# Optimization experiments

Measured on AMD Instinct MI355X. Metric: run time of the kernel, lower is better.

Reference implementation:

```python
import jax, jax.numpy as jnp
import numpy as np

LN_EPS = 1e-5

def _layer_norm(x, g, b):
    m = jnp.mean(x, axis=-1, keepdims=True)
    v = jnp.mean((x - m) ** 2, axis=-1, keepdims=True)
    return (x - m) / jnp.sqrt(v + LN_EPS) * g + b

def setup_inputs() -> dict:
    key = jax.random.key(0)
    ks = jax.random.split(key, 16)
    B, L, D = 4, 2048, 1024
    DF = 4 * D
    s_in = 1.0 / np.sqrt(D)
    s_ff = 1.0 / np.sqrt(DF)
    # torch init of phazor: exp(2j*pi*arange(D)/D) * |randn|
    ang = 2.0 * np.pi * jnp.arange(D, dtype=jnp.float32) / D
    mag = jnp.abs(jax.random.normal(ks[0], (D,), jnp.float32))
    return {
        "x": jax.random.normal(ks[1], (B, L, D), jnp.float32),
        "hidden_real": jax.random.normal(ks[2], (B, D), jnp.float32),
        "hidden_imag": jax.random.normal(ks[3], (B, D), jnp.float32),
        "phazor_real": mag * jnp.cos(ang),
        "phazor_imag": mag * jnp.sin(ang),
        "phazor_init_real": jax.random.normal(ks[4], (D,), jnp.float32),
        "phazor_init_imag": jax.random.normal(ks[5], (D,), jnp.float32),
        "ln_gamma": jnp.ones((D,), jnp.float32),
        "ln_beta": jnp.zeros((D,), jnp.float32),
        "fc_w": jax.random.uniform(ks[6], (D, D), jnp.float32, -s_in, s_in),
        "fc_b": jax.random.uniform(ks[7], (D,), jnp.float32, -s_in, s_in),
        "w1": jax.random.uniform(ks[8], (DF, D), jnp.float32, -s_in, s_in),
        "b1": jax.random.uniform(ks[9], (DF,), jnp.float32, -s_in, s_in),
        "w2": jax.random.uniform(ks[10], (D, DF), jnp.float32, -s_ff, s_ff),
        "b2": jax.random.uniform(ks[11], (D,), jnp.float32, -s_ff, s_ff),
    }

def _spiral_conv(x, hidden, phazor_p, phazor_init):
    # x: [B,L,D] real, hidden: [B,D] complex
    B, L, D = x.shape
    amag = jnp.abs(phazor_p)
    phazor = phazor_p / amag * jnp.exp(-amag)                      # [D]
    prog = jnp.power(phazor[None, :], jnp.arange(L)[:, None])      # [L,D]
    filt = prog * phazor_init[None, :]                             # [L,D]
    filt_fft = jnp.fft.fft(filt, n=2 * L, axis=0)                  # [2L,D]
    x_fft = jnp.fft.fft(x.astype(jnp.complex64), n=2 * L, axis=1)  # [B,2L,D]
    conv = jnp.fft.ifft(filt_fft[None] * x_fft, axis=1)[:, :L]     # [B,L,D]
    conv_with_past = conv + jax.lax.stop_gradient(hidden)[:, None, :] * prog[None] * phazor[None, None]
    return conv_with_past.real, conv_with_past

def reference(x, hidden_real, hidden_imag, phazor_real, phazor_imag,
              phazor_init_real, phazor_init_imag, ln_gamma, ln_beta,
              fc_w, fc_b, w1, b1, w2, b2):
    hidden = hidden_real + 1j * hidden_imag
    phazor_p = phazor_real + 1j * phazor_imag
    phazor_init = phazor_init_real + 1j * phazor_init_imag

    x_res = x
    xn = _layer_norm(x, ln_gamma, ln_beta)
    s, new_hidden = _spiral_conv(xn, hidden, phazor_p, phazor_init)
    y = jax.nn.silu(jnp.einsum('bld,ed->ble', x, fc_w) + fc_b)
    h = s * y + x_res                      # dropout is identity (p=0 / eval)
    hn = _layer_norm(h, ln_gamma, ln_beta) # same LayerNorm instance reused
    ffn = jnp.einsum('blf,df->bld', jax.nn.silu(jnp.einsum('bld,fd->blf', hn, w1) + b1), w2) + b2
    out = ffn + h
    return out, new_hidden
```

## Files before the change

kernel.cpp:

```cpp
#include <hip/hip_runtime.h>

typedef unsigned short u16;
typedef unsigned int u32;
typedef float f32x4 __attribute__((ext_vector_type(4)));
typedef __bf16 bf16x8 __attribute__((ext_vector_type(8)));

__device__ __forceinline__ float b2f(u16 u) {
    return __uint_as_float(((u32)u) << 16);
}
__device__ __forceinline__ u16 f2b(float f) {
    u32 u = __float_as_uint(f);
    return (u16)((u + 0x7FFFu + ((u >> 16) & 1u)) >> 16);
}
__device__ __forceinline__ bool is_f32(const u32* flag) {
    return flag[0] == 0x3F800000u;
}
__device__ __forceinline__ float lda(const void* p, size_t i, bool f) {
    return f ? ((const float*)p)[i] : b2f(((const u16*)p)[i]);
}
__device__ __forceinline__ void cmul(float& xr, float& xi, float yr, float yi) {
    float tr = xr * yr - xi * yi;
    xi = xr * yi + xi * yr;
    xr = tr;
}
__device__ __forceinline__ void gl2lds16(const void* g, void* l) {
    __builtin_amdgcn_global_load_lds(
        (const __attribute__((address_space(1))) void*)g,
        (__attribute__((address_space(3))) void*)l, 16, 0, 0);
}
__device__ __forceinline__ void wg_barrier() {
    asm volatile("" ::: "memory");
    __builtin_amdgcn_sched_barrier(0);
    __builtin_amdgcn_s_barrier();
    __builtin_amdgcn_sched_barrier(0);
    asm volatile("" ::: "memory");
}
#define VWAIT0 { asm volatile("s_waitcnt vmcnt(0)" ::: "memory"); __builtin_amdgcn_sched_barrier(0); }
#define VWAIT2 { asm volatile("s_waitcnt vmcnt(2)" ::: "memory"); __builtin_amdgcn_sched_barrier(0); }
#define VWAIT4 { asm volatile("s_waitcnt vmcnt(4)" ::: "memory"); __builtin_amdgcn_sched_barrier(0); }
#define LGKM0  { asm volatile("s_waitcnt lgkmcnt(0)" ::: "memory"); __builtin_amdgcn_sched_barrier(0); }

__global__ __launch_bounds__(256) void cvt_k(const void* __restrict__ src,
                                             u32* __restrict__ dst, int n2,
                                             const u32* __restrict__ flag) {
    bool f = is_f32(flag);
    int i = blockIdx.x * 256 + threadIdx.x;
    if (i >= n2) return;
    if (f) {
        float2 v = ((const float2*)src)[i];
        dst[i] = (u32)f2b(v.x) | ((u32)f2b(v.y) << 16);
    } else {
        dst[i] = ((const u32*)src)[i];
    }
}

__global__ __launch_bounds__(256) void ln_k(const u16* __restrict__ x,
                                            const u16* __restrict__ g,
                                            const u16* __restrict__ be,
                                            u16* __restrict__ o, int D) {
    int row = blockIdx.x;
    const u16* xr = x + (size_t)row * D;
    int tid = threadIdx.x;
    float s = 0.f, s2 = 0.f;
    for (int i = tid; i < D; i += 256) {
        float v = b2f(xr[i]);
        s += v; s2 += v * v;
    }
    for (int off = 32; off > 0; off >>= 1) {
        s  += __shfl_down(s,  off, 64);
        s2 += __shfl_down(s2, off, 64);
    }
    __shared__ float red[8];
    int wave = tid >> 6;
    if ((tid & 63) == 0) { red[wave * 2] = s; red[wave * 2 + 1] = s2; }
    __syncthreads();
    if (tid == 0) {
        float ts = 0.f, ts2 = 0.f;
        for (int w = 0; w < 4; w++) { ts += red[w * 2]; ts2 += red[w * 2 + 1]; }
        float m = ts / D;
        float v = ts2 / D - m * m;
        red[0] = m;
        red[1] = rsqrtf(v + 1e-5f);
    }
    __syncthreads();
    float m = red[0], inv = red[1];
    u16* orow = o + (size_t)row * D;
    for (int i = tid; i < D; i += 256) {
        float v = (b2f(xr[i]) - m) * inv * b2f(g[i]) + b2f(be[i]);
        orow[i] = f2b(v);
    }
}

__global__ __launch_bounds__(256) void scan_partial_k(const u16* __restrict__ xn,
                                                      const void* __restrict__ phr_,
                                                      const void* __restrict__ phi_,
                                                      float2* __restrict__ T,
                                                      int L, int D, int C, int Kc,
                                                      const u32* __restrict__ flag) {
    bool f = is_f32(flag);
    int tid = blockIdx.x * 256 + threadIdx.x;
    int d = tid % D;
    int c = (tid / D) % C;
    int b = tid / (D * C);
    float pr = lda(phr_, d, f), pi = lda(phi_, d, f);
    float amag = fmaxf(sqrtf(pr * pr + pi * pi), 1e-12f);
    float sc = __expf(-amag) / amag;
    float phr = pr * sc, phi = pi * sc;
    float Tr = 0.f, Ti = 0.f;
    const u16* xp = xn + ((size_t)b * L + (size_t)c * Kc) * D + d;
    for (int t = 0; t < Kc; t++) {
        float x = b2f(xp[(size_t)t * D]);
        float nr = phr * Tr - phi * Ti + x;
        Ti = phr * Ti + phi * Tr;
        Tr = nr;
    }
    T[tid] = make_float2(Tr, Ti);
}

__global__ __launch_bounds__(256) void scan_prefix_k(const void* __restrict__ phr_,
                                                     const void* __restrict__ phi_,
                                                     const float2* __restrict__ T,
                                                     float2* __restrict__ E,
                                                     int D, int C,
                                                     const u32* __restrict__ flag) {
    bool f = is_f32(flag);
    int tid = blockIdx.x * 256 + threadIdx.x;
    int d = tid % D;
    int b = tid / D;
    float pr = lda(phr_, d, f), pi = lda(phi_, d, f);
    float amag = fmaxf(sqrtf(pr * pr + pi * pi), 1e-12f);
    float sc = __expf(-amag) / amag;
    float phr = pr * sc, phi = pi * sc;
    float kr = phr, ki = phi;
    for (int s = 0; s < 7; s++) cmul(kr, ki, kr, ki);
    float cr = 0.f, ci = 0.f;
    for (int c = 0; c < C; c++) {
        size_t i = ((size_t)b * C + c) * D + d;
        E[i] = make_float2(cr, ci);
        float2 t = T[i];
        cmul(cr, ci, kr, ki);
        cr += t.x; ci += t.y;
    }
}

__global__ __launch_bounds__(256) void scan_final_k(const u16* __restrict__ xn,
                                                    const void* __restrict__ phr_,
                                                    const void* __restrict__ phi_,
                                                    const void* __restrict__ pir_,
                                                    const void* __restrict__ pii_,
                                                    const void* __restrict__ hr_,
                                                    const void* __restrict__ hi_,
                                                    const float2* __restrict__ E,
                                                    u16* __restrict__ sws,
                                                    void* __restrict__ dout,
                                                    int MD, int out_elems,
                                                    int L, int D, int C, int Kc,
                                                    const u32* __restrict__ flag) {
    bool f = is_f32(flag);
    int tid = blockIdx.x * 256 + threadIdx.x;
    int d = tid % D;
    int c = (tid / D) % C;
    int b = tid / (D * C);
    float pr = lda(phr_, d, f), pi = lda(phi_, d, f);
    float amag = fmaxf(sqrtf(pr * pr + pi * pi), 1e-12f);
    float sc = __expf(-amag) / amag;
    float phr = pr * sc, phi = pi * sc;
    float kr = phr, ki = phi;
    for (int s = 0; s < 7; s++) cmul(kr, ki, kr, ki);
    float Pr = phr, Pi = phi;
    for (int j = 0; j < c; j++) cmul(Pr, Pi, kr, ki);
    float ir = lda(pir_, d, f), ii = lda(pii_, d, f);
    float hr = lda(hr_, (size_t)b * D + d, f), hi = lda(hi_, (size_t)b * D + d, f);
    float2 e = E[tid];
    float Sr = e.x, Si = e.y;
    const bool full = (out_elems >= 3 * MD);
    size_t mbase = (size_t)b * L + (size_t)c * Kc;
    for (int t = 0; t < Kc; t++) {
        size_t off = (mbase + t) * D + d;
        float x = b2f(xn[off]);
        float nr = phr * Sr - phi * Si + x;
        Si = phr * Si + phi * Sr;
        Sr = nr;
        float cr = ir * Sr - ii * Si + hr * Pr - hi * Pi;
        float ci = ir * Si + ii * Sr + hr * Pi + hi * Pr;
        sws[off] = f2b(cr);
        if (f) {
            float* fo = (float*)dout;
            if (full) {
                fo[(size_t)MD + 2 * off]     = cr;
                fo[(size_t)MD + 2 * off + 1] = ci;
            } else {
                fo[(size_t)MD + off] = cr;
            }
        } else {
            u16* uo = (u16*)dout;
            if (full) {
                uo[(size_t)MD + 2 * off]     = f2b(cr);
                uo[(size_t)MD + 2 * off + 1] = f2b(ci);
            } else {
                uo[(size_t)MD + off] = f2b(cr);
            }
        }
        cmul(Pr, Pi, phr, phi);
    }
}

template <int MODE, int BN>
__global__ __launch_bounds__(512) void gemm_nt(const u16* __restrict__ A,
                                               const u16* __restrict__ Bm,
                                               int M, int N, int K,
                                               const u16* __restrict__ bias,
                                               const u16* __restrict__ sbuf,
                                               const u16* __restrict__ xbuf,
                                               u16* __restrict__ out,
                                               void* __restrict__ outv,
                                               const u32* __restrict__ flag) {
    constexpr int WN = BN / 4;
    constexpr int NB = BN / 64;
    __shared__ u16 As[2][256 * 64];
    __shared__ u16 Bs[2][BN * 64];
    const int tid = threadIdx.x;
    const int wave = tid >> 6, lane = tid & 63;
    const int quad = lane >> 4, l16 = lane & 15;

    const int NT = N / BN;
    const int j = blockIdx.x;
    const int gsize = 8 * NT;
    const int mg  = j / gsize;
    const int rem = j - mg * gsize;
    const int nt  = rem >> 3;
    const int mi  = rem & 7;
    const int bm = (mg * 8 + mi) * 256, bn = nt * BN;

    const int wrow = (wave >> 2) * 128, wcol = (wave & 3) * WN;

    f32x4 acc[8][NB] = {};

    const int lr = lane >> 3;
    const int sl = (lane & 7) ^ lr;
    const size_t goff = (size_t)lr * K + sl * 8;
    const u16* aG = A  + (size_t)(bm + wave * 16) * K + goff;
    const u16* bG = Bm + (size_t)(bn + wave * 16) * K + goff;
    const size_t K8 = (size_t)K * 8;

#define STG_A(B_, t_, h_) { \
        const u16* ga = aG + (size_t)(t_) * 64 + (size_t)(h_) * 128 * K; \
        gl2lds16(ga,      &As[B_][((h_) * 128 + wave * 16) * 64]); \
        gl2lds16(ga + K8, &As[B_][((h_) * 128 + wave * 16 + 8) * 64]); }
#define STG_B(B_, t_, h_) { \
        const u16* gb = bG + (size_t)(t_) * 64 + (size_t)(h_) * 128 * K; \
        gl2lds16(gb,      &Bs[B_][((h_) * 128 + wave * 16) * 64]); \
        gl2lds16(gb + K8, &Bs[B_][((h_) * 128 + wave * 16 + 8) * 64]); }

#define RDA(B_, m_, ks_) (*(const bf16x8*)&As[B_][(wrow + (m_) * 16 + l16) * 64 + \
        ((((ks_) * 4 + quad) ^ (l16 & 7)) << 3)])
#define RDB(B_, n_, ks_) (*(const bf16x8*)&Bs[B_][(wcol + (n_) * 16 + l16) * 64 + \
        ((((ks_) * 4 + quad) ^ (l16 & 7)) << 3)])

#define LDA4(RB, mh) { \
        av[0][0] = RDA(RB, (mh) * 4 + 0, 0); av[0][1] = RDA(RB, (mh) * 4 + 0, 1); \
        av[1][0] = RDA(RB, (mh) * 4 + 1, 0); av[1][1] = RDA(RB, (mh) * 4 + 1, 1); \
        av[2][0] = RDA(RB, (mh) * 4 + 2, 0); av[2][1] = RDA(RB, (mh) * 4 + 2, 1); \
        av[3][0] = RDA(RB, (mh) * 4 + 3, 0); av[3][1] = RDA(RB, (mh) * 4 + 3, 1); }
#define LDB2(RB, nh) { \
        bv[(nh) * 2 + 0][0] = RDB(RB, (nh) * 2 + 0, 0); \
        bv[(nh) * 2 + 0][1] = RDB(RB, (nh) * 2 + 0, 1); \
        bv[(nh) * 2 + 1][0] = RDB(RB, (nh) * 2 + 1, 0); \
        bv[(nh) * 2 + 1][1] = RDB(RB, (nh) * 2 + 1, 1); }

#define FM(mi_, ni_, ks_) acc[mi_][ni_] = __builtin_amdgcn_mfma_f32_16x16x32_bf16( \
        av[(mi_) & 3][ks_], bv[ni_][ks_], acc[mi_][ni_], 0, 0, 0)
#define MFMA16(mh, nh) { \
        __builtin_amdgcn_s_setprio(1); \
        FM((mh)*4+0, (nh)*2+0, 0); FM((mh)*4+0, (nh)*2+1, 0); \
        FM((mh)*4+1, (nh)*2+0, 0); FM((mh)*4+1, (nh)*2+1, 0); \
        FM((mh)*4+2, (nh)*2+0, 0); FM((mh)*4+2, (nh)*2+1, 0); \
        FM((mh)*4+3, (nh)*2+0, 0); FM((mh)*4+3, (nh)*2+1, 0); \
        FM((mh)*4+0, (nh)*2+0, 1); FM((mh)*4+0, (nh)*2+1, 1); \
        FM((mh)*4+1, (nh)*2+0, 1); FM((mh)*4+1, (nh)*2+1, 1); \
        FM((mh)*4+2, (nh)*2+0, 1); FM((mh)*4+2, (nh)*2+1, 1); \
        FM((mh)*4+3, (nh)*2+0, 1); FM((mh)*4+3, (nh)*2+1, 1); \
        __builtin_amdgcn_s_setprio(0); }

    bf16x8 av[4][2], bv[NB][2];
    const int KT = K >> 6;

    if constexpr (BN == 256) {
        STG_A(0, 0, 0); STG_B(0, 0, 0); STG_B(0, 0, 1); STG_A(0, 0, 1);
        VWAIT4; wg_barrier();
#define TILE256(RB, SB, t_) { \
        const bool stg = (t_) + 1 < KT; \
         \
        LDA4(RB, 0); LDB2(RB, 0); \
        if (stg) STG_A(SB, (t_) + 1, 0);       \
        wg_barrier(); LGKM0; \
        MFMA16(0, 0); \
        if (stg) { VWAIT4 } else { VWAIT2 }    \
        wg_barrier(); \
         \
        LDB2(RB, 1); \
        if (stg) STG_B(SB, (t_) + 1, 0);       \
        wg_barrier(); LGKM0; \
        MFMA16(0, 1); \
        if (stg) { VWAIT4 } else { VWAIT0 }    \
        wg_barrier(); \
         \
        LDA4(RB, 1); \
        if (stg) STG_B(SB, (t_) + 1, 1);       \
        wg_barrier(); LGKM0; \
        MFMA16(1, 0); \
        wg_barrier(); \
         \
        if (stg) STG_A(SB, (t_) + 1, 1);       \
        wg_barrier(); LGKM0; \
        MFMA16(1, 1); \
        if (stg) { VWAIT4 }                    \
        wg_barrier(); }
        for (int t = 0; t < KT; t += 2) {
            TILE256(0, 1, t);
            TILE256(1, 0, t + 1);
        }
#undef TILE256
    } else {
        STG_B(0, 0, 0); STG_A(0, 0, 0); STG_A(0, 0, 1);
        VWAIT2; wg_barrier();
#define TILE128(RB, SB, t_) { \
        const bool stg = (t_) + 1 < KT; \
         \
        LDA4(RB, 0); LDB2(RB, 0); \
        if (stg) { STG_B(SB, (t_) + 1, 0); STG_A(SB, (t_) + 1, 0); }  \
        wg_barrier(); LGKM0; \
        MFMA16(0, 0); \
        if (stg) { VWAIT4 } else { VWAIT0 }    \
        wg_barrier(); \
         \
        LDA4(RB, 1); \
        if (stg) STG_A(SB, (t_) + 1, 1);       \
        wg_barrier(); LGKM0; \
        MFMA16(1, 0); \
        if (stg) { VWAIT2 }                    \
        wg_barrier(); }
        for (int t = 0; t < KT; t += 2) {
            TILE128(0, 1, t);
            TILE128(1, 0, t + 1);
        }
#undef TILE128
    }

    bool f = (MODE == 2) ? is_f32(flag) : false;
#pragma unroll
    for (int m = 0; m < 8; m++) {
#pragma unroll
        for (int n = 0; n < NB; n++) {
            int colg = bn + wcol + n * 16 + l16;
            float bsv = b2f(bias[colg]);
#pragma unroll
            for (int r = 0; r < 4; r++) {
                int rowg = bm + wrow + m * 16 + quad * 4 + r;
                size_t idx = (size_t)rowg * N + colg;
                float v = acc[m][n][r] + bsv;
                if (MODE == 0) {
                    float y = v / (1.f + __expf(-v));
                    float hv = b2f(sbuf[idx]) * y + b2f(xbuf[idx]);
                    out[idx] = f2b(hv);
                } else if (MODE == 1) {
                    float y = v / (1.f + __expf(-v));
                    out[idx] = f2b(y);
                } else {
                    float o = v + b2f(xbuf[idx]);
                    if (f) ((float*)outv)[idx] = o;
                    else   ((u16*)outv)[idx] = f2b(o);
                }
            }
        }
    }
#undef STG_A
#undef STG_B
#undef RDA
#undef RDB
#undef LDA4
#undef LDB2
#undef FM
#undef MFMA16
}

extern "C" void kernel_launch(void* const* d_in, const int* in_sizes, int n_in,
                              void* d_out, int out_size, void* d_ws, size_t ws_size,
                              hipStream_t stream) {
    const void* x   = d_in[0];
    const void* hr  = d_in[1];
    const void* hi  = d_in[2];
    const void* phr = d_in[3];
    const void* phi = d_in[4];
    const void* pir = d_in[5];
    const void* pii = d_in[6];
    const void* g   = d_in[7];
    const void* be  = d_in[8];
    const void* fcw = d_in[9];
    const void* fcb = d_in[10];
    const void* w1  = d_in[11];
    const void* b1  = d_in[12];
    const void* w2  = d_in[13];
    const void* b2  = d_in[14];
    const u32* flag = (const u32*)g;

    const int D  = in_sizes[3];
    const int Bb = in_sizes[1] / D;
    const int L  = in_sizes[0] / (Bb * D);
    const int DF = in_sizes[12];
    const int M  = Bb * L;
    const int Kc = 128, C = L / Kc;
    const int MD = M * D;

    char* ws = (char*)d_ws;
    size_t MD2 = (size_t)MD * 2;
    u16*    xb  = (u16*)(ws);
    u16*    xn  = (u16*)(ws + MD2);
    u16*    sws = (u16*)(ws + 2 * MD2);
    float2* T   = (float2*)(ws + 3 * MD2);
    float2* E   = (float2*)(ws + 3 * MD2 + (size_t)Bb * C * D * 8);
    u16*    a1  = (u16*)(ws);
    u16*    h   = (u16*)(ws + 4 * MD2);
    u16*    hn  = (u16*)(ws + 5 * MD2);
    char*   wp  = ws + 6 * MD2;
    u16* fcwb = (u16*)wp; wp += (size_t)D * D * 2;
    u16* w1b  = (u16*)wp; wp += (size_t)DF * D * 2;
    u16* w2b  = (u16*)wp; wp += (size_t)D * DF * 2;
    u16* fcbb = (u16*)wp; wp += (size_t)D * 2;
    u16* b1b  = (u16*)wp; wp += (size_t)DF * 2;
    u16* b2b  = (u16*)wp; wp += (size_t)D * 2;
    u16* gb   = (u16*)wp; wp += (size_t)D * 2;
    u16* bb   = (u16*)wp; wp += (size_t)D * 2;

    auto cvt = [&](const void* src, u16* dst, size_t n) {
        int n2 = (int)(n / 2);
        cvt_k<<<(n2 + 255) / 256, 256, 0, stream>>>(src, (u32*)dst, n2, flag);
    };
    cvt(x,   xb,   (size_t)MD);
    cvt(fcw, fcwb, (size_t)D * D);
    cvt(w1,  w1b,  (size_t)DF * D);
    cvt(w2,  w2b,  (size_t)D * DF);
    cvt(fcb, fcbb, (size_t)D);
    cvt(b1,  b1b,  (size_t)DF);
    cvt(b2,  b2b,  (size_t)D);
    cvt(g,   gb,   (size_t)D);
    cvt(be,  bb,   (size_t)D);

    ln_k<<<M, 256, 0, stream>>>(xb, gb, bb, xn, D);
    scan_partial_k<<<(Bb * C * D) / 256, 256, 0, stream>>>(xn, phr, phi, T, L, D, C, Kc, flag);
    scan_prefix_k<<<(Bb * D) / 256, 256, 0, stream>>>(phr, phi, T, E, D, C, flag);
    scan_final_k<<<(Bb * C * D) / 256, 256, 0, stream>>>(xn, phr, phi, pir, pii, hr, hi,
                                                         E, sws, d_out, MD, out_size,
                                                         L, D, C, Kc, flag);
    gemm_nt<0, 128><<<(M / 256) * (D / 128), 512, 0, stream>>>(xb, fcwb, M, D, D, fcbb, sws, xb, h, nullptr, flag);
    ln_k<<<M, 256, 0, stream>>>(h, gb, bb, hn, D);
    gemm_nt<1, 256><<<(M / 256) * (DF / 256), 512, 0, stream>>>(hn, w1b, M, DF, D, b1b, nullptr, nullptr, a1, nullptr, flag);
    gemm_nt<2, 128><<<(M / 256) * (D / 128), 512, 0, stream>>>(a1, w2b, M, D, DF, b2b, nullptr, h, nullptr, d_out, flag);
}
```

Measured before the change: 466.4 us.

## Triple-buffer BN=128 GEMM path and merge conversion launches into one kernel

The BN=128 GEMM variant now uses a 2x4 wave grid with 64x64 per-wave tiles and a three-stage LDS ring, so loads are issued two K-tiles ahead instead of one. This is meant to hide more global-load latency in the fc and w2 GEMMs. It costs more LDS per block, which may lower occupancy, and the new buffer rotation is more complex. Separately, the nine conversion kernel launches become a single multi-segment kernel. That removes launch overhead but adds a per-thread segment search loop.

```diff
diff --git a/kernel.cpp b/kernel.cpp
--- a/kernel.cpp
+++ b/kernel.cpp
@@ -38,19 +38,27 @@
 #define VWAIT0 { asm volatile("s_waitcnt vmcnt(0)" ::: "memory"); __builtin_amdgcn_sched_barrier(0); }
 #define VWAIT2 { asm volatile("s_waitcnt vmcnt(2)" ::: "memory"); __builtin_amdgcn_sched_barrier(0); }
 #define VWAIT4 { asm volatile("s_waitcnt vmcnt(4)" ::: "memory"); __builtin_amdgcn_sched_barrier(0); }
+#define VWAIT6 { asm volatile("s_waitcnt vmcnt(6)" ::: "memory"); __builtin_amdgcn_sched_barrier(0); }
 #define LGKM0  { asm volatile("s_waitcnt lgkmcnt(0)" ::: "memory"); __builtin_amdgcn_sched_barrier(0); }
 
-__global__ __launch_bounds__(256) void cvt_k(const void* __restrict__ src,
-                                             u32* __restrict__ dst, int n2,
-                                             const u32* __restrict__ flag) {
+struct CvtArgs {
+    const void* src[9];
+    u16* dst[9];
+    int n2[9];
+    int tot;
+};
+__global__ __launch_bounds__(256) void cvtm_k(CvtArgs a, const u32* __restrict__ flag) {
     bool f = is_f32(flag);
     int i = blockIdx.x * 256 + threadIdx.x;
-    if (i >= n2) return;
+    if (i >= a.tot) return;
+    int s = 0, base = 0;
+    while (i - base >= a.n2[s]) { base += a.n2[s]; s++; }
+    int k = i - base;
     if (f) {
-        float2 v = ((const float2*)src)[i];
-        dst[i] = (u32)f2b(v.x) | ((u32)f2b(v.y) << 16);
+        float2 v = ((const float2*)a.src[s])[k];
+        ((u32*)a.dst[s])[k] = (u32)f2b(v.x) | ((u32)f2b(v.y) << 16);
     } else {
-        dst[i] = ((const u32*)src)[i];
+        ((u32*)a.dst[s])[k] = ((const u32*)a.src[s])[k];
     }
 }
 
@@ -215,10 +223,10 @@
                                                u16* __restrict__ out,
                                                void* __restrict__ outv,
                                                const u32* __restrict__ flag) {
-    constexpr int WN = BN / 4;
-    constexpr int NB = BN / 64;
-    __shared__ u16 As[2][256 * 64];
-    __shared__ u16 Bs[2][BN * 64];
+    constexpr int NBUF = (BN == 256) ? 2 : 3;
+    constexpr int MR   = (BN == 256) ? 8 : 4;
+    __shared__ u16 As[NBUF][256 * 64];
+    __shared__ u16 Bs[NBUF][BN * 64];
     const int tid = threadIdx.x;
     const int wave = tid >> 6, lane = tid & 63;
     const int quad = lane >> 4, l16 = lane & 15;
@@ -232,16 +240,17 @@
     const int mi  = rem & 7;
     const int bm = (mg * 8 + mi) * 256, bn = nt * BN;
 
-    const int wrow = (wave >> 2) * 128, wcol = (wave & 3) * WN;
-
-    f32x4 acc[8][NB] = {};
+    const int wrow = (BN == 256) ? (wave >> 2) * 128 : (wave >> 1) * 64;
+    const int wcol = (BN == 256) ? (wave & 3) * 64   : (wave & 1) * 64;
+
+    f32x4 acc[MR][4] = {};
 
     const int lr = lane >> 3;
     const int sl = (lane & 7) ^ lr;
     const size_t goff = (size_t)lr * K + sl * 8;
-    const u16* aG = A  + (size_t)(bm + wave * 16) * K + goff;
+    const size_t K8 = (size_t)K * 8;
+    const u16* aG = A  + (size_t)(bm + ((BN == 256) ? wave * 16 : wave * 32)) * K + goff;
     const u16* bG = Bm + (size_t)(bn + wave * 16) * K + goff;
-    const size_t K8 = (size_t)K * 8;
 
 #define STG_A(B_, t_, h_) { \
         const u16* ga = aG + (size_t)(t_) * 64 + (size_t)(h_) * 128 * K; \
@@ -251,6 +260,16 @@
         const u16* gb = bG + (size_t)(t_) * 64 + (size_t)(h_) * 128 * K; \
         gl2lds16(gb,      &Bs[B_][((h_) * 128 + wave * 16) * 64]); \
         gl2lds16(gb + K8, &Bs[B_][((h_) * 128 + wave * 16 + 8) * 64]); }
+#define STG_A128(B_, t_) { \
+        const u16* ga = aG + (size_t)(t_) * 64; \
+        gl2lds16(ga,          &As[B_][(wave * 32) * 64]); \
+        gl2lds16(ga + K8,     &As[B_][(wave * 32 + 8) * 64]); \
+        gl2lds16(ga + 2 * K8, &As[B_][(wave * 32 + 16) * 64]); \
+        gl2lds16(ga + 3 * K8, &As[B_][(wave * 32 + 24) * 64]); }
+#define STG_B128(B_, t_) { \
+        const u16* gb = bG + (size_t)(t_) * 64; \
+        gl2lds16(gb,      &Bs[B_][(wave * 16) * 64]); \
+        gl2lds16(gb + K8, &Bs[B_][(wave * 16 + 8) * 64]); }
 
 #define RDA(B_, m_, ks_) (*(const bf16x8*)&As[B_][(wrow + (m_) * 16 + l16) * 64 + \
         ((((ks_) * 4 + quad) ^ (l16 & 7)) << 3)])
@@ -281,8 +300,15 @@
         FM((mh)*4+2, (nh)*2+0, 1); FM((mh)*4+2, (nh)*2+1, 1); \
         FM((mh)*4+3, (nh)*2+0, 1); FM((mh)*4+3, (nh)*2+1, 1); \
         __builtin_amdgcn_s_setprio(0); }
-
-    bf16x8 av[4][2], bv[NB][2];
+#define MFMA16K(ks_) { \
+        __builtin_amdgcn_s_setprio(1); \
+        FM(0, 0, ks_); FM(0, 1, ks_); FM(1, 0, ks_); FM(1, 1, ks_); \
+        FM(0, 2, ks_); FM(0, 3, ks_); FM(1, 2, ks_); FM(1, 3, ks_); \
+        FM(2, 0, ks_); FM(2, 1, ks_); FM(3, 0, ks_); FM(3, 1, ks_); \
+        FM(2, 2, ks_); FM(2, 3, ks_); FM(3, 2, ks_); FM(3, 3, ks_); \
+        __builtin_amdgcn_s_setprio(0); }
+
+    bf16x8 av[4][2], bv[4][2];
     const int KT = K >> 6;
 
     if constexpr (BN == 256) {
@@ -322,36 +348,45 @@
         }
 #undef TILE256
     } else {
-        STG_B(0, 0, 0); STG_A(0, 0, 0); STG_A(0, 0, 1);
-        VWAIT2; wg_barrier();
+        STG_A128(0, 0); STG_B128(0, 0);
+        STG_A128(1, 1); STG_B128(1, 1);
+        VWAIT6;
+        wg_barrier();
 #define TILE128(RB, SB, t_) { \
-        const bool stg = (t_) + 1 < KT; \
-         \
-        LDA4(RB, 0); LDB2(RB, 0); \
-        if (stg) { STG_B(SB, (t_) + 1, 0); STG_A(SB, (t_) + 1, 0); }  \
-        wg_barrier(); LGKM0; \
-        MFMA16(0, 0); \
-        if (stg) { VWAIT4 } else { VWAIT0 }    \
+        const bool stg = (t_) + 2 < KT; \
+         \
+        av[0][0] = RDA(RB, 0, 0); av[1][0] = RDA(RB, 1, 0); \
+        av[2][0] = RDA(RB, 2, 0); av[3][0] = RDA(RB, 3, 0); \
+        bv[0][0] = RDB(RB, 0, 0); bv[1][0] = RDB(RB, 1, 0); \
+        bv[2][0] = RDB(RB, 2, 0); bv[3][0] = RDB(RB, 3, 0); \
+        if (stg) STG_A128(SB, (t_) + 2); \
+        wg_barrier(); LGKM0; \
+        MFMA16K(0); \
         wg_barrier(); \
          \
-        LDA4(RB, 1); \
-        if (stg) STG_A(SB, (t_) + 1, 1);       \
-        wg_barrier(); LGKM0; \
-        MFMA16(1, 0); \
-        if (stg) { VWAIT2 }                    \
+        av[0][1] = RDA(RB, 0, 1); av[1][1] = RDA(RB, 1, 1); \
+        av[2][1] = RDA(RB, 2, 1); av[3][1] = RDA(RB, 3, 1); \
+        bv[0][1] = RDB(RB, 0, 1); bv[1][1] = RDB(RB, 1, 1); \
+        bv[2][1] = RDB(RB, 2, 1); bv[3][1] = RDB(RB, 3, 1); \
+        if (stg) STG_B128(SB, (t_) + 2); \
+        wg_barrier(); LGKM0; \
+        MFMA16K(1); \
+        if (stg) { VWAIT6 }                    \
+        else if ((t_) + 1 < KT) { VWAIT0 }     \
         wg_barrier(); }
-        for (int t = 0; t < KT; t += 2) {
-            TILE128(0, 1, t);
-            TILE128(1, 0, t + 1);
+        for (int t = 0; t < KT; t += 3) {
+            TILE128(0, 2, t);
+            if (t + 1 < KT) TILE128(1, 0, t + 1);
+            if (t + 2 < KT) TILE128(2, 1, t + 2);
         }
 #undef TILE128
     }
 
     bool f = (MODE == 2) ? is_f32(flag) : false;
 #pragma unroll
-    for (int m = 0; m < 8; m++) {
+    for (int m = 0; m < MR; m++) {
 #pragma unroll
-        for (int n = 0; n < NB; n++) {
+        for (int n = 0; n < 4; n++) {
             int colg = bn + wcol + n * 16 + l16;
             float bsv = b2f(bias[colg]);
 #pragma unroll
@@ -376,12 +411,15 @@
     }
 #undef STG_A
 #undef STG_B
+#undef STG_A128
+#undef STG_B128
 #undef RDA
 #undef RDB
 #undef LDA4
 #undef LDB2
 #undef FM
 #undef MFMA16
+#undef MFMA16K
 }
 
 extern "C" void kernel_launch(void* const* d_in, const int* in_sizes, int n_in,
@@ -432,19 +470,20 @@
     u16* gb   = (u16*)wp; wp += (size_t)D * 2;
     u16* bb   = (u16*)wp; wp += (size_t)D * 2;
 
-    auto cvt = [&](const void* src, u16* dst, size_t n) {
-        int n2 = (int)(n / 2);
-        cvt_k<<<(n2 + 255) / 256, 256, 0, stream>>>(src, (u32*)dst, n2, flag);
-    };
-    cvt(x,   xb,   (size_t)MD);
-    cvt(fcw, fcwb, (size_t)D * D);
-    cvt(w1,  w1b,  (size_t)DF * D);
-    cvt(w2,  w2b,  (size_t)D * DF);
-    cvt(fcb, fcbb, (size_t)D);
-    cvt(b1,  b1b,  (size_t)DF);
-    cvt(b2,  b2b,  (size_t)D);
-    cvt(g,   gb,   (size_t)D);
-    cvt(be,  bb,   (size_t)D);
+    CvtArgs ca;
+    const void* srcs[9] = { x, fcw, w1, w2, fcb, b1, b2, g, be };
+    u16* dsts[9] = { xb, fcwb, w1b, w2b, fcbb, b1b, b2b, gb, bb };
+    size_t ns[9] = { (size_t)MD, (size_t)D * D, (size_t)DF * D, (size_t)D * DF,
+                     (size_t)D, (size_t)DF, (size_t)D, (size_t)D, (size_t)D };
+    int tot = 0;
+    for (int i = 0; i < 9; i++) {
+        ca.src[i] = srcs[i];
+        ca.dst[i] = dsts[i];
+        ca.n2[i] = (int)(ns[i] / 2);
+        tot += ca.n2[i];
+    }
+    ca.tot = tot;
+    cvtm_k<<<(tot + 255) / 256, 256, 0, stream>>>(ca, flag);
 
     ln_k<<<M, 256, 0, stream>>>(xb, gb, bb, xn, D);
     scan_partial_k<<<(Bb * C * D) / 256, 256, 0, stream>>>(xn, phr, phi, T, L, D, C, Kc, flag);
```

New measurement: 462.8 us. Within noise of the previous version (-0.8%).
